# Kernel optimization log

Measured on AMD Instinct MI355X. Metric: run time of the kernel, lower is better.

## Reference

```python
import jax, jax.numpy as jnp
import numpy as np

T, B, H, W, D, N, M, A = 48, 16, 16, 48, 684, 256, 256, 512
CQ, KQ, PAD = 512, 11, 5  # coverage conv: 1->512 channels, 11x11, pad 5


def setup_inputs() -> dict:
    key = jax.random.key(0)
    ks = iter(jax.random.split(key, 40))
    w = lambda *s: jax.random.normal(next(ks), s, jnp.float32) * 0.05
    inp = {
        "embedding": jax.random.normal(next(ks), (T, B, M), jnp.float32),
        "mask": jnp.ones((T, B), jnp.float32),
        "context": jax.random.normal(next(ks), (B, D, H, W), jnp.float32),
        "context_mask": jnp.ones((B, H, W), jnp.float32),
        "init_state": jax.random.normal(next(ks), (B, N), jnp.float32),
        # attention params
        "Ua_w": w(A, D), "Ua_b": w(A),              # conv_Ua (1x1 conv == linear over channels)
        "Wa_w": w(A, N),                              # fc_Wa (no bias)
        "Q_w": w(CQ, 1, KQ, KQ),                      # conv_Q (no bias)
        "Uf_w": w(A, CQ), "Uf_b": w(A),               # fc_Uf
        "va_w": w(1, A), "va_b": w(1),                # fc_va
        # GRU 1 (input-driven)
        "Wyz_w": w(N, M), "Wyz_b": w(N),
        "Wyr_w": w(N, M), "Wyr_b": w(N),
        "Wyh_w": w(N, M), "Wyh_b": w(N),
        "Uhz_w": w(N, N), "Uhr_w": w(N, N), "Uhh_w": w(N, N),
        # GRU 2 (context-driven)
        "Wcz_w": w(N, D), "Wcr_w": w(N, D), "Wch_w": w(N, D),
        "Uhz2_w": w(N, N), "Uhz2_b": w(N),
        "Uhr2_w": w(N, N), "Uhr2_b": w(N),
        "Uhh2_w": w(N, N), "Uhh2_b": w(N),
    }
    return inp


def reference(embedding, mask, context, context_mask, init_state,
              Ua_w, Ua_b, Wa_w, Q_w, Uf_w, Uf_b, va_w, va_b,
              Wyz_w, Wyz_b, Wyr_w, Wyr_b, Wyh_w, Wyh_b,
              Uhz_w, Uhr_w, Uhh_w, Wcz_w, Wcr_w, Wch_w,
              Uhz2_w, Uhz2_b, Uhr2_w, Uhr2_b, Uhh2_w, Uhh2_b):
    # Precompute, as the torch module does, the context projection and
    # embedding projections for all steps.
    Ua_ctx = jnp.einsum('bdhw,ad->hwba', context, Ua_w) + Ua_b   # [H,W,B,A]
    sz = jnp.einsum('tbm,nm->tbn', embedding, Wyz_w) + Wyz_b     # [T,B,N]
    sr = jnp.einsum('tbm,nm->tbn', embedding, Wyr_w) + Wyr_b
    sh = jnp.einsum('tbm,nm->tbn', embedding, Wyh_w) + Wyh_b
    ctx_mask_hwb = jnp.transpose(context_mask, (1, 2, 0))        # [H,W,B]
    nb = context.shape[0]
    alpha_past0 = jnp.zeros((nb, context.shape[2], context.shape[3]), context.dtype)

    def step(carry, xs):
        h, ap = carry
        m_t, sz_t, sr_t, sh_t = xs
        # GRU 1
        z1 = jax.nn.sigmoid(h @ Uhz_w.T + sz_t)
        r1 = jax.nn.sigmoid(h @ Uhr_w.T + sr_t)
        h1p = jnp.tanh((h @ Uhh_w.T) * r1 + sh_t)
        h1 = z1 * h + (1.0 - z1) * h1p
        h1 = m_t[:, None] * h1 + (1.0 - m_t)[:, None] * h
        # coverage-conv attention
        Wa_h1 = h1 @ Wa_w.T                                      # [B,A]
        cf = jax.lax.conv_general_dilated(
            ap[:, None], Q_w, (1, 1), [(PAD, PAD), (PAD, PAD)],
            dimension_numbers=('NCHW', 'OIHW', 'NCHW'))          # [B,CQ,H,W]
        cover = jnp.einsum('bchw,ac->hwba', cf, Uf_w) + Uf_b     # [H,W,B,A]
        att = jnp.tanh(Ua_ctx + Wa_h1[None, None] + cover)
        e = jnp.einsum('hwba,a->hwb', att, va_w[0]) + va_b[0]
        alpha = jnp.exp(e) * ctx_mask_hwb
        alpha = alpha / alpha.sum(axis=(0, 1))[None, None, :]    # normalize over H,W
        a_bhw = jnp.transpose(alpha, (2, 0, 1))
        ap_new = ap + a_bhw
        ct = jnp.einsum('bdhw,bhw->bd', context, a_bhw)          # [B,D]
        # GRU 2
        z2 = jax.nn.sigmoid(ct @ Wcz_w.T + h1 @ Uhz2_w.T + Uhz2_b)
        r2 = jax.nn.sigmoid(ct @ Wcr_w.T + h1 @ Uhr2_w.T + Uhr2_b)
        h2p = jnp.tanh(ct @ Wch_w.T + (h1 @ Uhh2_w.T + Uhh2_b) * r2)
        h2 = z2 * h1 + (1.0 - z2) * h2p
        h2 = m_t[:, None] * h2 + (1.0 - m_t)[:, None] * h1
        return (h2, ap_new), (h2, ct, a_bhw, ap_new)

    _, (h2ts, cts, alphas, alpha_pasts) = jax.lax.scan(
        step, (init_state, alpha_past0), (mask, sz, sr, sh))
    return h2ts, cts, alphas, alpha_pasts
```

## Files before the change

### kernel.cpp

```cpp
#include <hip/hip_runtime.h>
#include <hip/hip_bf16.h>
#include <stdint.h>

#define T_  48
#define B_  16
#define HW_ 768
#define D_  684
#define N_  256
#define A_  512

#define OFF_SZ     0u
#define OFF_SR     196608u
#define OFF_SH     393216u
#define OFF_UHZT   589824u
#define OFF_UHZ2T  786432u
#define OFF_G2HP   983040u
#define OFF_WAT    1179648u
#define OFF_WCZT   1310720u
#define OFF_UAB    1836032u
#define OFF_WAHP   2012160u
#define OFF_H1     2077696u
#define OFF_KCB    2186240u
#define OFF_G2CT   2219008u
#define OFF_AP     2275008u
#define OFF_AUN    2287296u
#define OFF_UACTX  2299584u

#define OUT_H2 0u
#define OUT_CT 196608u
#define OUT_AL 721920u
#define OUT_AP 1311744u

typedef __attribute__((ext_vector_type(8))) short bf16x8;
typedef __attribute__((ext_vector_type(16))) float floatx16;

__device__ __forceinline__ float sigf(float x)  { return 1.f / (1.f + __expf(-x)); }
__device__ __forceinline__ float tanhf_(float x){ float e = __expf(2.f*x); return 1.f - 2.f/(e + 1.f); }
__device__ __forceinline__ float bfval(unsigned short u){ return __uint_as_float(((unsigned)u) << 16); }
__device__ __forceinline__ unsigned short f2bf(float f){
  unsigned int x = __float_as_uint(f);
  return (unsigned short)((x + 0x7fffu + ((x >> 16) & 1u)) >> 16);
}

__global__ void k_prep(const float* __restrict__ Uhz, const float* __restrict__ Uhr, const float* __restrict__ Uhh,
                       const float* __restrict__ Uhz2, const float* __restrict__ Uhr2, const float* __restrict__ Uhh2,
                       const float* __restrict__ Wyz, const float* __restrict__ Wyr, const float* __restrict__ Wyh,
                       const float* __restrict__ Wa, const float* __restrict__ Wcz, const float* __restrict__ Wcr,
                       const float* __restrict__ Wch, const float* __restrict__ Ua, float* __restrict__ ws)
{
  int i = blockIdx.x * 256 + threadIdx.x;
  if (i < 589824) {
    int m = i >> 16, rem = i & 65535, r = rem >> 8, c = rem & 255;
    const float* s;
    unsigned dst;
    switch (m) { case 0: s=Uhz;  dst=OFF_UHZT;           break;
                 case 1: s=Uhr;  dst=OFF_UHZT+65536u;    break;
                 case 2: s=Uhh;  dst=OFF_UHZT+131072u;   break;
                 case 3: s=Uhz2; dst=OFF_UHZ2T;          break;
                 case 4: s=Uhr2; dst=OFF_UHZ2T+65536u;   break;
                 case 5: s=Uhh2; dst=OFF_UHZ2T+131072u;  break;
                 case 6: s=Wyz;  dst=983040u;            break;
                 case 7: s=Wyr;  dst=1048576u;           break;
                 default: s=Wyh; dst=1114112u;           break;}
    ws[dst + c*256 + r] = s[rem];
  } else if (i < 720896) {
    int j = i - 589824, r = j >> 8, c = j & 255;
    ws[OFF_WAT + c*512 + r] = Wa[j];
  } else if (i < 1246208) {
    int j = i - 720896; int m = j / 175104; int rem = j - m*175104;
    int r = rem / 684, c = rem - r*684;
    const float* s = (m == 0) ? Wcz : (m == 1) ? Wcr : Wch;
    ws[OFF_WCZT + m*175104 + c*256 + r] = s[rem];
  } else if (i < 1596416) {
    int j = i - 1246208; int a = j / 684, d = j - a*684;
    unsigned short* uab = (unsigned short*)(ws + OFF_UAB);
    uab[(size_t)a*688 + d] = f2bf(Ua[j]);
  } else if (i < 1598464) {
    int j = i - 1596416; int a = j >> 2, d = 684 + (j & 3);
    unsigned short* uab = (unsigned short*)(ws + OFF_UAB);
    uab[(size_t)a*688 + d] = 0;
  } else if (i < 1610752) {
    ws[OFF_AP + (i - 1598464)] = 0.f;
  }
}

__global__ void __launch_bounds__(256) k_kcomb(const float* __restrict__ Uf, const float* __restrict__ Qw,
                                               float* __restrict__ ws)
{
  unsigned short* kcb = (unsigned short*)(ws + OFF_KCB);
  int tid = threadIdx.x;
  int k = tid & 127, rr = tid >> 7;
  int a = blockIdx.x * 2 + rr;
  if (k >= 121) { kcb[(size_t)a*128 + k] = 0; return; }
  const float* uf = Uf + (size_t)a*512;
  float acc = 0.f;
  #pragma unroll 8
  for (int c = 0; c < 512; ++c) acc += uf[c] * Qw[c*121 + k];
  kcb[(size_t)a*128 + k] = f2bf(acc);
}

__global__ void __launch_bounds__(256) k_embproj(const float* __restrict__ emb, const float* __restrict__ bz,
                                                 const float* __restrict__ br, const float* __restrict__ bh,
                                                 float* __restrict__ ws)
{
  __shared__ __align__(16) float s_e[256 * 16];
  __shared__ float s_part[8][32][48];
  int tid = threadIdx.x;
  int rc = blockIdx.x >> 3, cc = blockIdx.x & 7;
  int row0 = rc * 16, n0 = cc * 32;
  for (int i = tid; i < 4096; i += 256) { int r = i >> 8, m = i & 255; s_e[m*16 + r] = emb[(row0 + r)*256 + m]; }
  __syncthreads();
  int col = tid & 31, kg = tid >> 5;
  int n = n0 + col;
  float az[16], ar[16], ah[16];
  #pragma unroll
  for (int r = 0; r < 16; ++r) { az[r] = 0.f; ar[r] = 0.f; ah[r] = 0.f; }
  #pragma unroll 4
  for (int m = kg*32; m < kg*32 + 32; ++m) {
    float wz = ws[983040u + m*256 + n];
    float wr = ws[1048576u + m*256 + n];
    float wh = ws[1114112u + m*256 + n];
    const float4* ep = (const float4*)(s_e + m*16);
    #pragma unroll
    for (int rq = 0; rq < 4; ++rq) {
      float4 e4 = ep[rq];
      az[rq*4+0] += wz*e4.x; az[rq*4+1] += wz*e4.y; az[rq*4+2] += wz*e4.z; az[rq*4+3] += wz*e4.w;
      ar[rq*4+0] += wr*e4.x; ar[rq*4+1] += wr*e4.y; ar[rq*4+2] += wr*e4.z; ar[rq*4+3] += wr*e4.w;
      ah[rq*4+0] += wh*e4.x; ah[rq*4+1] += wh*e4.y; ah[rq*4+2] += wh*e4.z; ah[rq*4+3] += wh*e4.w;
    }
  }
  #pragma unroll
  for (int r = 0; r < 16; ++r) {
    s_part[kg][col][r]      = az[r];
    s_part[kg][col][16 + r] = ar[r];
    s_part[kg][col][32 + r] = ah[r];
  }
  __syncthreads();
  {
    int rcol = tid & 31, j0 = (tid >> 5) * 6;
    int rn = n0 + rcol;
    #pragma unroll
    for (int jj = 0; jj < 6; ++jj) {
      int j = j0 + jj;
      float v = 0.f;
      #pragma unroll
      for (int k8 = 0; k8 < 8; ++k8) v += s_part[k8][rcol][j];
      int g = j >> 4, r = j & 15;
      const float* bp = (g == 0) ? bz : (g == 1) ? br : bh;
      v += bp[rn];
      ws[g*196608u + (row0 + r)*256 + rn] = v;
    }
  }
}

__global__ void __launch_bounds__(256) k_uactx(const float* __restrict__ ctx, float* __restrict__ ws)
{
  __shared__ unsigned short sA[32 * 24];
  int tid = threadIdx.x;
  int blk = blockIdx.x;
  int b = blk / 48; int r2 = blk % 48; int ch = r2 >> 1; int ah = r2 & 1;
  int hw0 = ch * 32;
  const unsigned short* uab = (const unsigned short*)(ws + OFF_UAB);
  int lane = tid & 63, w = tid >> 6;
  int c5 = lane & 31, q = lane >> 5;
  int nb = ah*256 + w*64;
  floatx16 acc[2];
  #pragma unroll
  for (int nt = 0; nt < 2; ++nt)
    #pragma unroll
    for (int r = 0; r < 16; ++r) acc[nt][r] = 0.f;
  int dd = tid >> 4, iw = tid & 15;
  for (int kt = 0; kt < 43; ++kt) {
    int d = kt*16 + dd;
    float2 v = {0.f, 0.f};
    if (d < 684) v = *(const float2*)(ctx + ((size_t)(b*684 + d))*768 + hw0 + iw*2);
    __syncthreads();
    sA[(iw*2 + 0)*24 + dd] = f2bf(v.x);
    sA[(iw*2 + 1)*24 + dd] = f2bf(v.y);
    __syncthreads();
    bf16x8 af = *(const bf16x8*)(sA + c5*24 + q*8);
    #pragma unroll
    for (int nt = 0; nt < 2; ++nt) {
      bf16x8 bf = *(const bf16x8*)(uab + (size_t)(nb + nt*32 + c5)*688 + kt*16 + q*8);
      acc[nt] = __builtin_amdgcn_mfma_f32_32x32x16_bf16(af, bf, acc[nt], 0, 0, 0);
    }
  }
  unsigned short* up = (unsigned short*)(ws + OFF_UACTX);
  #pragma unroll
  for (int nt = 0; nt < 2; ++nt) {
    int col = nb + nt*32 + c5;
    #pragma unroll
    for (int r = 0; r < 16; ++r) {
      int row32 = (r & 3) + 8*(r >> 2) + 4*q;
      int hw = hw0 + row32;
      up[((size_t)(b*768 + hw))*512 + col] = f2bf(acc[nt][r]);
    }
  }
}

__global__ void __launch_bounds__(256) k_step0(const float* __restrict__ inits, const float* __restrict__ maskp,
                                               float* __restrict__ ws)
{
  __shared__ float s_h[256];
  __shared__ float s_part[3][8][32];
  __shared__ float s_h1[32];
  int tid = threadIdx.x;
  int b = blockIdx.x >> 3, q = blockIdx.x & 7;
  s_h[tid] = inits[b*256 + tid];
  if (q == 0) {
    for (int i = tid; i < 768; i += 256) ws[OFF_AUN + b*768 + i] = 0.f;
    #pragma unroll
    for (int g = 0; g < 3; ++g) ws[OFF_G2CT + (b*3 + g)*256 + tid] = 0.f;
  }
  __syncthreads();
  {
    int nl = tid & 31, kq = tid >> 5;
    int col = q*32 + nl;
    const float* Wz = ws + OFF_UHZT;
    const float* Wr = ws + OFF_UHZT + 65536u;
    const float* Wh = ws + OFF_UHZT + 131072u;
    float a0 = 0.f, a1 = 0.f, a2 = 0.f;
    #pragma unroll 8
    for (int k = kq*32; k < kq*32 + 32; ++k) {
      float hk = s_h[k];
      a0 += Wz[k*256 + col]*hk; a1 += Wr[k*256 + col]*hk; a2 += Wh[k*256 + col]*hk;
    }
    s_part[0][kq][nl] = a0; s_part[1][kq][nl] = a1; s_part[2][kq][nl] = a2;
  }
  __syncthreads();
  if (tid < 32) {
    float g0 = 0.f, g1 = 0.f, g2 = 0.f;
    #pragma unroll
    for (int j = 0; j < 8; ++j) { g0 += s_part[0][j][tid]; g1 += s_part[1][j][tid]; g2 += s_part[2][j][tid]; }
    int col = q*32 + tid;
    int ro = b*256 + col;
    float z1 = sigf(g0 + ws[OFF_SZ + ro]);
    float r1 = sigf(g1 + ws[OFF_SR + ro]);
    float h1p = tanhf_(g2 * r1 + ws[OFF_SH + ro]);
    float m = maskp[b];
    float h = s_h[col];
    float h1 = m*(z1*h + (1.f - z1)*h1p) + (1.f - m)*h;
    s_h1[tid] = h1;
    ws[OFF_H1 + b*256 + col] = h1;
  }
  __syncthreads();
  {
    float acc0 = 0.f, acc1 = 0.f;
    #pragma unroll 8
    for (int j = 0; j < 32; ++j) {
      float h1j = s_h1[j];
      acc0 += ws[OFF_WAT + (q*32 + j)*512 + tid]       * h1j;
      acc1 += ws[OFF_WAT + (q*32 + j)*512 + tid + 256] * h1j;
    }
    ws[OFF_WAHP + (size_t)(b*8 + q)*512 + tid]       = acc0;
    ws[OFF_WAHP + (size_t)(b*8 + q)*512 + tid + 256] = acc1;
  }
  #pragma unroll
  for (int g = 0; g < 3; ++g) {
    const float* Wb = ws + OFF_UHZ2T + g*65536u;
    float acc = 0.f;
    #pragma unroll 8
    for (int j = 0; j < 32; ++j) acc += Wb[(q*32 + j)*256 + tid] * s_h1[j];
    ws[OFF_G2HP + (size_t)((b*8 + q)*3 + g)*256 + tid] = acc;
  }
}

__global__ void __launch_bounds__(256) k_step1(int t, const float* __restrict__ maskp,
                                               const float* __restrict__ bz2, const float* __restrict__ br2,
                                               const float* __restrict__ bh2,
                                               float* __restrict__ out, float* __restrict__ ws)
{
  __shared__ float s_h[256];
  __shared__ float s_part[3][8][32];
  __shared__ float s_h1[32];
  int tid = threadIdx.x;
  int b = blockIdx.x >> 3, q = blockIdx.x & 7;
  const unsigned pr = (unsigned)((t - 1) & 1);
  const unsigned pw = (unsigned)(t & 1);
  {
    int n = tid;
    float h1v = ws[OFF_H1 + pr*4096u + b*256 + n];
    float gz = ws[OFF_G2CT + pr*12288u + (b*3 + 0)*256 + n];
    float gr = ws[OFF_G2CT + pr*12288u + (b*3 + 1)*256 + n];
    float gc = ws[OFF_G2CT + pr*12288u + (b*3 + 2)*256 + n];
    float gu = 0.f;
    #pragma unroll
    for (int qq = 0; qq < 8; ++qq) {
      gz += ws[OFF_G2HP + pr*98304u + (size_t)((b*8 + qq)*3 + 0)*256 + n];
      gr += ws[OFF_G2HP + pr*98304u + (size_t)((b*8 + qq)*3 + 1)*256 + n];
      gu += ws[OFF_G2HP + pr*98304u + (size_t)((b*8 + qq)*3 + 2)*256 + n];
    }
    float z2 = sigf(gz + bz2[n]);
    float r2 = sigf(gr + br2[n]);
    float h2p = tanhf_(gc + (gu + bh2[n]) * r2);
    float h2 = z2*h1v + (1.f - z2)*h2p;
    float m = maskp[(t-1)*16 + b];
    float hv = m*h2 + (1.f - m)*h1v;
    if (q == 0) out[OUT_H2 + (size_t)((t-1)*16 + b)*256 + n] = hv;
    s_h[n] = hv;
  }
  if (q == 0) {
    for (int i = tid; i < 768; i += 256) ws[OFF_AUN + b*768 + i] = 0.f;
    #pragma unroll
    for (int g = 0; g < 3; ++g) ws[OFF_G2CT + pw*12288u + (b*3 + g)*256 + tid] = 0.f;
  }
  __syncthreads();
  {
    int nl = tid & 31, kq = tid >> 5;
    int col = q*32 + nl;
    const float* Wz = ws + OFF_UHZT;
    const float* Wr = ws + OFF_UHZT + 65536u;
    const float* Wh = ws + OFF_UHZT + 131072u;
    float a0 = 0.f, a1 = 0.f, a2 = 0.f;
    #pragma unroll 8
    for (int k = kq*32; k < kq*32 + 32; ++k) {
      float hk = s_h[k];
      a0 += Wz[k*256 + col]*hk; a1 += Wr[k*256 + col]*hk; a2 += Wh[k*256 + col]*hk;
    }
    s_part[0][kq][nl] = a0; s_part[1][kq][nl] = a1; s_part[2][kq][nl] = a2;
  }
  __syncthreads();
  if (tid < 32) {
    float g0 = 0.f, g1 = 0.f, g2 = 0.f;
    #pragma unroll
    for (int j = 0; j < 8; ++j) { g0 += s_part[0][j][tid]; g1 += s_part[1][j][tid]; g2 += s_part[2][j][tid]; }
    int col = q*32 + tid;
    int ro = (t*16 + b)*256 + col;
    float z1 = sigf(g0 + ws[OFF_SZ + ro]);
    float r1 = sigf(g1 + ws[OFF_SR + ro]);
    float h1p = tanhf_(g2 * r1 + ws[OFF_SH + ro]);
    float m = maskp[t*16 + b];
    float h = s_h[col];
    float h1 = m*(z1*h + (1.f - z1)*h1p) + (1.f - m)*h;
    s_h1[tid] = h1;
    ws[OFF_H1 + pw*4096u + b*256 + col] = h1;
  }
  __syncthreads();
  {
    float acc0 = 0.f, acc1 = 0.f;
    #pragma unroll 8
    for (int j = 0; j < 32; ++j) {
      float h1j = s_h1[j];
      acc0 += ws[OFF_WAT + (q*32 + j)*512 + tid]       * h1j;
      acc1 += ws[OFF_WAT + (q*32 + j)*512 + tid + 256] * h1j;
    }
    ws[OFF_WAHP + (size_t)(b*8 + q)*512 + tid]       = acc0;
    ws[OFF_WAHP + (size_t)(b*8 + q)*512 + tid + 256] = acc1;
  }
  #pragma unroll
  for (int g = 0; g < 3; ++g) {
    const float* Wb = ws + OFF_UHZ2T + g*65536u;
    float acc = 0.f;
    #pragma unroll 8
    for (int j = 0; j < 32; ++j) acc += Wb[(q*32 + j)*256 + tid] * s_h1[j];
    ws[OFF_G2HP + pw*98304u + (size_t)((b*8 + q)*3 + g)*256 + tid] = acc;
  }
}

__global__ void __launch_bounds__(256) k_cover(const float* __restrict__ va,
                                               const float* __restrict__ Uab, const float* __restrict__ Ufb,
                                               float* __restrict__ ws)
{
  __shared__ unsigned short sA[64 * 136];
  __shared__ float sWah[512];
  __shared__ float sVa[512];
  int tid = threadIdx.x;
  int blk = blockIdx.x;
  int b = blk / 24; int chA = blk % 24; int mt = chA >> 1; int nt2 = chA & 1;
  for (int i = tid; i < 512; i += 256) {
    float v = Uab[i] + Ufb[i];
    #pragma unroll
    for (int qq = 0; qq < 8; ++qq) v += ws[OFF_WAHP + (size_t)(b*8 + qq)*512 + i];
    sWah[i] = v; sVa[i] = va[i];
  }
  const float* ap = ws + OFF_AP + b*768;
  for (int idx = tid; idx < 64*128; idx += 256) {
    int r = idx & 63, k = idx >> 6;
    int hw = mt*64 + r; int hh = hw / 48; int wwp = hw - hh*48;
    float v = 0.f;
    if (k < 121) {
      int kh = k / 11, kw = k - kh*11;
      int shh = hh + kh - 5, sww = wwp + kw - 5;
      if (shh >= 0 && shh < 16 && sww >= 0 && sww < 48) v = ap[shh*48 + sww];
    }
    sA[r*136 + k] = f2bf(v);
  }
  __syncthreads();
  int lane = tid & 63; int w = tid >> 6; int mw = w >> 1; int nw = w & 1;
  int c5 = lane & 31; int q = lane >> 5;
  bf16x8 af[8];
  {
    int m = mw*32 + c5;
    #pragma unroll
    for (int ks = 0; ks < 8; ++ks)
      af[ks] = *(const bf16x8*)(sA + m*136 + ks*16 + q*8);
  }
  const unsigned short* kct = (const unsigned short*)(ws + OFF_KCB);
  const unsigned short* uact = (const unsigned short*)(ws + OFF_UACTX);
  float e_part[16];
  #pragma unroll
  for (int r = 0; r < 16; ++r) e_part[r] = 0.f;
  for (int sp = 0; sp < 2; ++sp) {
    int n_base = nt2*256 + nw*128 + sp*64;
    floatx16 acc[2];
    #pragma unroll
    for (int r = 0; r < 16; ++r) { acc[0][r] = 0.f; acc[1][r] = 0.f; }
    const bf16x8* kb0 = (const bf16x8*)(kct + (size_t)(n_base + c5)*128 + q*8);
    const bf16x8* kb1 = (const bf16x8*)(kct + (size_t)(n_base + 32 + c5)*128 + q*8);
    #pragma unroll
    for (int ks = 0; ks < 8; ++ks) {
      bf16x8 b0 = kb0[ks*2];
      bf16x8 b1 = kb1[ks*2];
      acc[0] = __builtin_amdgcn_mfma_f32_32x32x16_bf16(af[ks], b0, acc[0], 0, 0, 0);
      acc[1] = __builtin_amdgcn_mfma_f32_32x32x16_bf16(af[ks], b1, acc[1], 0, 0, 0);
    }
    #pragma unroll
    for (int half = 0; half < 2; ++half) {
      int col = n_base + half*32 + c5;
      float vav = sVa[col], wah = sWah[col];
      #pragma unroll
      for (int r = 0; r < 16; ++r) {
        int row32 = (r & 3) + 8*(r >> 2) + 4*q;
        int hw = mt*64 + mw*32 + row32;
        float x = acc[half][r] + wah + bfval(uact[((size_t)(b*768 + hw))*512 + col]);
        e_part[r] += vav * tanhf_(x);
      }
    }
  }
  #pragma unroll
  for (int r = 0; r < 16; ++r) {
    float v = e_part[r];
    v += __shfl_xor(v, 1); v += __shfl_xor(v, 2); v += __shfl_xor(v, 4);
    v += __shfl_xor(v, 8); v += __shfl_xor(v, 16);
    e_part[r] = v;
  }
  if (c5 == 0) {
    #pragma unroll
    for (int r = 0; r < 16; ++r) {
      int row32 = (r & 3) + 8*(r >> 2) + 4*q;
      int hw = mt*64 + mw*32 + row32;
      atomicAdd(&ws[OFF_AUN + b*768 + hw], e_part[r]);
    }
  }
}

__global__ void __launch_bounds__(256) k_alpha(int t, const float* __restrict__ ctx, const float* __restrict__ cmask,
                                               const float* __restrict__ vab,
                                               float* __restrict__ out, float* __restrict__ ws)
{
  __shared__ __align__(16) float s_al[768];
  __shared__ float s_red[4];
  __shared__ float s_ct[32];
  int tid = threadIdx.x;
  int b = blockIdx.x / 22, dc = blockIdx.x % 22;
  const unsigned pw = (unsigned)(t & 1);
  float vb = vab[0];
  float local = 0.f;
  for (int i = tid; i < 768; i += 256) {
    float e = ws[OFF_AUN + b*768 + i] + vb;
    float un = __expf(e) * cmask[b*768 + i];
    s_al[i] = un; local += un;
  }
  local += __shfl_xor(local, 1); local += __shfl_xor(local, 2); local += __shfl_xor(local, 4);
  local += __shfl_xor(local, 8); local += __shfl_xor(local, 16); local += __shfl_xor(local, 32);
  if ((tid & 63) == 0) s_red[tid >> 6] = local;
  __syncthreads();
  float inv = 1.f / (s_red[0] + s_red[1] + s_red[2] + s_red[3]);
  if (dc == 0) {
    float* outA = out + OUT_AL + (size_t)(t*16 + b)*768;
    float* outP = out + OUT_AP + (size_t)(t*16 + b)*768;
    for (int i = tid; i < 768; i += 256) {
      float av = s_al[i] * inv;
      float np = ws[OFF_AP + b*768 + i] + av;
      ws[OFF_AP + b*768 + i] = np;
      outA[i] = av; outP[i] = np;
    }
  }
  {
    int dl = tid >> 3, qq = tid & 7;
    int d = dc*32 + dl;
    if (d < 684) {
      const float4* cp  = (const float4*)(ctx + ((size_t)(b*684 + d))*768);
      const float4* alp = (const float4*)s_al;
      float s = 0.f;
      #pragma unroll 8
      for (int i = 0; i < 24; ++i) {
        float4 cv = cp[i*8 + qq]; float4 av = alp[i*8 + qq];
        s += cv.x*av.x + cv.y*av.y + cv.z*av.z + cv.w*av.w;
      }
      s += __shfl_xor(s, 1); s += __shfl_xor(s, 2); s += __shfl_xor(s, 4);
      s *= inv;
      if (qq == 0) {
        out[OUT_CT + (size_t)(t*16 + b)*684 + d] = s;
        s_ct[dl] = s;
      }
    } else if (qq == 0) {
      s_ct[dl] = 0.f;
    }
  }
  __syncthreads();
  {
    int d0 = dc*32;
    int jm = 684 - d0; if (jm > 32) jm = 32;
    #pragma unroll
    for (int g = 0; g < 3; ++g) {
      const float* Wb = ws + OFF_WCZT + g*175104u;
      float acc = 0.f;
      for (int j = 0; j < jm; ++j) acc += Wb[(d0 + j)*256 + tid] * s_ct[j];
      atomicAdd(&ws[OFF_G2CT + pw*12288u + (size_t)(b*3 + g)*256 + tid], acc);
    }
  }
}

__global__ void k_final(const float* __restrict__ maskp, const float* __restrict__ bz2,
                        const float* __restrict__ br2, const float* __restrict__ bh2,
                        float* __restrict__ out, float* __restrict__ ws)
{
  int b = blockIdx.x, n = threadIdx.x;
  const unsigned pr = 1u;
  float h1v = ws[OFF_H1 + pr*4096u + b*256 + n];
  float gz = ws[OFF_G2CT + pr*12288u + (b*3 + 0)*256 + n];
  float gr = ws[OFF_G2CT + pr*12288u + (b*3 + 1)*256 + n];
  float gc = ws[OFF_G2CT + pr*12288u + (b*3 + 2)*256 + n];
  float gu = 0.f;
  #pragma unroll
  for (int qq = 0; qq < 8; ++qq) {
    gz += ws[OFF_G2HP + pr*98304u + (size_t)((b*8 + qq)*3 + 0)*256 + n];
    gr += ws[OFF_G2HP + pr*98304u + (size_t)((b*8 + qq)*3 + 1)*256 + n];
    gu += ws[OFF_G2HP + pr*98304u + (size_t)((b*8 + qq)*3 + 2)*256 + n];
  }
  float z2 = sigf(gz + bz2[n]);
  float r2 = sigf(gr + br2[n]);
  float h2p = tanhf_(gc + (gu + bh2[n]) * r2);
  float h2 = z2*h1v + (1.f - z2)*h2p;
  float m = maskp[47*16 + b];
  out[OUT_H2 + (size_t)(47*16 + b)*256 + n] = m*h2 + (1.f - m)*h1v;
}

extern "C" void kernel_launch(void* const* d_in, const int* in_sizes, int n_in,
                              void* d_out, int out_size, void* d_ws, size_t ws_size,
                              hipStream_t stream)
{
  const float* emb   = (const float*)d_in[0];
  const float* maskp = (const float*)d_in[1];
  const float* ctx   = (const float*)d_in[2];
  const float* cmask = (const float*)d_in[3];
  const float* inits = (const float*)d_in[4];
  const float* Ua    = (const float*)d_in[5];
  const float* Uab   = (const float*)d_in[6];
  const float* Wa    = (const float*)d_in[7];
  const float* Qw    = (const float*)d_in[8];
  const float* Uf    = (const float*)d_in[9];
  const float* Ufb   = (const float*)d_in[10];
  const float* va    = (const float*)d_in[11];
  const float* vab   = (const float*)d_in[12];
  const float* Wyz   = (const float*)d_in[13];
  const float* Wyzb  = (const float*)d_in[14];
  const float* Wyr   = (const float*)d_in[15];
  const float* Wyrb  = (const float*)d_in[16];
  const float* Wyh   = (const float*)d_in[17];
  const float* Wyhb  = (const float*)d_in[18];
  const float* Uhz   = (const float*)d_in[19];
  const float* Uhr   = (const float*)d_in[20];
  const float* Uhh   = (const float*)d_in[21];
  const float* Wcz   = (const float*)d_in[22];
  const float* Wcr   = (const float*)d_in[23];
  const float* Wch   = (const float*)d_in[24];
  const float* Uhz2  = (const float*)d_in[25];
  const float* Uhz2b = (const float*)d_in[26];
  const float* Uhr2  = (const float*)d_in[27];
  const float* Uhr2b = (const float*)d_in[28];
  const float* Uhh2  = (const float*)d_in[29];
  const float* Uhh2b = (const float*)d_in[30];
  float* out = (float*)d_out;
  float* ws  = (float*)d_ws;

  k_prep<<<dim3(6292), dim3(256), 0, stream>>>(Uhz, Uhr, Uhh, Uhz2, Uhr2, Uhh2,
                                               Wyz, Wyr, Wyh, Wa, Wcz, Wcr, Wch, Ua, ws);
  k_kcomb<<<dim3(256), dim3(256), 0, stream>>>(Uf, Qw, ws);
  k_embproj<<<dim3(384), dim3(256), 0, stream>>>(emb, Wyzb, Wyrb, Wyhb, ws);
  k_uactx<<<dim3(768), dim3(256), 0, stream>>>(ctx, ws);
  k_step0<<<dim3(128), dim3(256), 0, stream>>>(inits, maskp, ws);

  k_cover<<<dim3(384), dim3(256), 0, stream>>>(va, Uab, Ufb, ws);
  k_alpha<<<dim3(352), dim3(256), 0, stream>>>(0, ctx, cmask, vab, out, ws);
  for (int t = 1; t < 48; ++t) {
    k_step1<<<dim3(128), dim3(256), 0, stream>>>(t, maskp, Uhz2b, Uhr2b, Uhh2b, out, ws);
    k_cover<<<dim3(384), dim3(256), 0, stream>>>(va, Uab, Ufb, ws);
    k_alpha<<<dim3(352), dim3(256), 0, stream>>>(t, ctx, cmask, vab, out, ws);
  }
  k_final<<<dim3(16), dim3(256), 0, stream>>>(maskp, Uhz2b, Uhr2b, Uhh2b, out, ws);
  (void)in_sizes; (void)n_in; (void)out_size; (void)ws_size;
}
```

Measured before the change: 2.473 ms.

## Fuse per-step kernels into one persistent kernel with per-batch grid barriers

Replaces the 144 per-timestep kernel launches (step, cover, alpha) with a single persistent kernel of 384 blocks. Each batch element gets 24 blocks, and they synchronize through an atomic counter barrier in workspace between phases. This removes launch overhead and the full-device serialization between dependent kernels. The risks are deadlock if not all blocks are co-resident, spin-wait cost, and idle blocks in phases that use only 8 or 22 of the 24 blocks.

Measured after the change: 6.602 ms. 167% more time.

```diff
diff --git a/kernel.cpp b/kernel.cpp
--- a/kernel.cpp
+++ b/kernel.cpp
@@ -20,6 +20,7 @@
 #define OFF_UAB    1836032u
 #define OFF_WAHP   2012160u
 #define OFF_H1     2077696u
+#define OFF_BAR    2085888u
 #define OFF_KCB    2186240u
 #define OFF_G2CT   2219008u
 #define OFF_AP     2275008u
@@ -81,6 +82,8 @@
     uab[(size_t)a*688 + d] = 0;
   } else if (i < 1610752) {
     ws[OFF_AP + (i - 1598464)] = 0.f;
+  } else if (i < 1611008) {
+    ws[OFF_BAR + (i - 1610752)] = 0.f;
   }
 }
 
@@ -198,87 +201,275 @@
   }
 }
 
-__global__ void __launch_bounds__(256) k_step0(const float* __restrict__ inits, const float* __restrict__ maskp,
-                                               float* __restrict__ ws)
+__global__ void __launch_bounds__(256, 2) k_loop(
+    const float* __restrict__ inits, const float* __restrict__ maskp,
+    const float* __restrict__ bz2, const float* __restrict__ br2, const float* __restrict__ bh2,
+    const float* __restrict__ va, const float* __restrict__ Uab, const float* __restrict__ Ufb,
+    const float* __restrict__ ctx, const float* __restrict__ cmask, const float* __restrict__ vab,
+    float* __restrict__ out, float* ws)
 {
-  __shared__ float s_h[256];
-  __shared__ float s_part[3][8][32];
-  __shared__ float s_h1[32];
+  __shared__ union {
+    struct { float s_h[256]; float s_part[3][8][32]; float s_h1[32]; } p1;
+    struct { unsigned short sA[64*136]; float sWah[512]; float sVa[512]; } p2;
+    struct { __align__(16) float s_al[768]; float s_red[4]; float s_ct[32]; } p3;
+  } u;
   int tid = threadIdx.x;
-  int b = blockIdx.x >> 3, q = blockIdx.x & 7;
-  s_h[tid] = inits[b*256 + tid];
-  if (q == 0) {
-    for (int i = tid; i < 768; i += 256) ws[OFF_AUN + b*768 + i] = 0.f;
-    #pragma unroll
-    for (int g = 0; g < 3; ++g) ws[OFF_G2CT + (b*3 + g)*256 + tid] = 0.f;
-  }
-  __syncthreads();
-  {
-    int nl = tid & 31, kq = tid >> 5;
-    int col = q*32 + nl;
-    const float* Wz = ws + OFF_UHZT;
-    const float* Wr = ws + OFF_UHZT + 65536u;
-    const float* Wh = ws + OFF_UHZT + 131072u;
-    float a0 = 0.f, a1 = 0.f, a2 = 0.f;
-    #pragma unroll 8
-    for (int k = kq*32; k < kq*32 + 32; ++k) {
-      float hk = s_h[k];
-      a0 += Wz[k*256 + col]*hk; a1 += Wr[k*256 + col]*hk; a2 += Wh[k*256 + col]*hk;
-    }
-    s_part[0][kq][nl] = a0; s_part[1][kq][nl] = a1; s_part[2][kq][nl] = a2;
-  }
-  __syncthreads();
-  if (tid < 32) {
-    float g0 = 0.f, g1 = 0.f, g2 = 0.f;
-    #pragma unroll
-    for (int j = 0; j < 8; ++j) { g0 += s_part[0][j][tid]; g1 += s_part[1][j][tid]; g2 += s_part[2][j][tid]; }
-    int col = q*32 + tid;
-    int ro = b*256 + col;
-    float z1 = sigf(g0 + ws[OFF_SZ + ro]);
-    float r1 = sigf(g1 + ws[OFF_SR + ro]);
-    float h1p = tanhf_(g2 * r1 + ws[OFF_SH + ro]);
-    float m = maskp[b];
-    float h = s_h[col];
-    float h1 = m*(z1*h + (1.f - z1)*h1p) + (1.f - m)*h;
-    s_h1[tid] = h1;
-    ws[OFF_H1 + b*256 + col] = h1;
-  }
-  __syncthreads();
-  {
-    float acc0 = 0.f, acc1 = 0.f;
-    #pragma unroll 8
-    for (int j = 0; j < 32; ++j) {
-      float h1j = s_h1[j];
-      acc0 += ws[OFF_WAT + (q*32 + j)*512 + tid]       * h1j;
-      acc1 += ws[OFF_WAT + (q*32 + j)*512 + tid + 256] * h1j;
-    }
-    ws[OFF_WAHP + (size_t)(b*8 + q)*512 + tid]       = acc0;
-    ws[OFF_WAHP + (size_t)(b*8 + q)*512 + tid + 256] = acc1;
-  }
-  #pragma unroll
-  for (int g = 0; g < 3; ++g) {
-    const float* Wb = ws + OFF_UHZ2T + g*65536u;
-    float acc = 0.f;
-    #pragma unroll 8
-    for (int j = 0; j < 32; ++j) acc += Wb[(q*32 + j)*256 + tid] * s_h1[j];
-    ws[OFF_G2HP + (size_t)((b*8 + q)*3 + g)*256 + tid] = acc;
-  }
-}
-
-__global__ void __launch_bounds__(256) k_step1(int t, const float* __restrict__ maskp,
-                                               const float* __restrict__ bz2, const float* __restrict__ br2,
-                                               const float* __restrict__ bh2,
-                                               float* __restrict__ out, float* __restrict__ ws)
-{
-  __shared__ float s_h[256];
-  __shared__ float s_part[3][8][32];
-  __shared__ float s_h1[32];
-  int tid = threadIdx.x;
-  int b = blockIdx.x >> 3, q = blockIdx.x & 7;
-  const unsigned pr = (unsigned)((t - 1) & 1);
-  const unsigned pw = (unsigned)(t & 1);
-  {
+  int b = blockIdx.x / 24, j = blockIdx.x % 24;
+  unsigned* bar = (unsigned*)(ws + OFF_BAR) + b*16;
+  unsigned bk = 0;
+
+#define GBAR() do { \
+    __syncthreads(); \
+    if (tid == 0) { \
+      __threadfence(); \
+      __hip_atomic_fetch_add(bar, 1u, __ATOMIC_RELAXED, __HIP_MEMORY_SCOPE_AGENT); \
+      bk += 24u; \
+      while (__hip_atomic_load(bar, __ATOMIC_RELAXED, __HIP_MEMORY_SCOPE_AGENT) < bk) \
+        __builtin_amdgcn_s_sleep(4); \
+      __threadfence(); \
+    } \
+    __syncthreads(); \
+  } while (0)
+
+  for (int t = 0; t < 48; ++t) {
+    if (j < 8) {
+      int q = j;
+      if (t == 0) {
+        u.p1.s_h[tid] = inits[b*256 + tid];
+        if (q == 0) {
+          for (int i = tid; i < 768; i += 256) ws[OFF_AUN + b*768 + i] = 0.f;
+          #pragma unroll
+          for (int g = 0; g < 3; ++g) ws[OFF_G2CT + (b*3 + g)*256 + tid] = 0.f;
+        }
+        __syncthreads();
+      } else {
+        const unsigned pr = (unsigned)((t - 1) & 1);
+        const unsigned pw = (unsigned)(t & 1);
+        {
+          int n = tid;
+          float h1v = ws[OFF_H1 + pr*4096u + b*256 + n];
+          float gz = ws[OFF_G2CT + pr*12288u + (b*3 + 0)*256 + n];
+          float gr = ws[OFF_G2CT + pr*12288u + (b*3 + 1)*256 + n];
+          float gc = ws[OFF_G2CT + pr*12288u + (b*3 + 2)*256 + n];
+          float gu = 0.f;
+          #pragma unroll
+          for (int qq = 0; qq < 8; ++qq) {
+            gz += ws[OFF_G2HP + pr*98304u + (size_t)((b*8 + qq)*3 + 0)*256 + n];
+            gr += ws[OFF_G2HP + pr*98304u + (size_t)((b*8 + qq)*3 + 1)*256 + n];
+            gu += ws[OFF_G2HP + pr*98304u + (size_t)((b*8 + qq)*3 + 2)*256 + n];
+          }
+          float z2 = sigf(gz + bz2[n]);
+          float r2 = sigf(gr + br2[n]);
+          float h2p = tanhf_(gc + (gu + bh2[n]) * r2);
+          float h2 = z2*h1v + (1.f - z2)*h2p;
+          float m = maskp[(t-1)*16 + b];
+          float hv = m*h2 + (1.f - m)*h1v;
+          if (q == 0) out[OUT_H2 + (size_t)((t-1)*16 + b)*256 + n] = hv;
+          u.p1.s_h[n] = hv;
+        }
+        if (q == 0) {
+          for (int i = tid; i < 768; i += 256) ws[OFF_AUN + b*768 + i] = 0.f;
+          #pragma unroll
+          for (int g = 0; g < 3; ++g) ws[OFF_G2CT + pw*12288u + (b*3 + g)*256 + tid] = 0.f;
+        }
+        __syncthreads();
+      }
+      {
+        int nl = tid & 31, kq = tid >> 5;
+        int col = q*32 + nl;
+        const float* Wz = ws + OFF_UHZT;
+        const float* Wr = ws + OFF_UHZT + 65536u;
+        const float* Wh = ws + OFF_UHZT + 131072u;
+        float a0 = 0.f, a1 = 0.f, a2 = 0.f;
+        #pragma unroll 8
+        for (int k = kq*32; k < kq*32 + 32; ++k) {
+          float hk = u.p1.s_h[k];
+          a0 += Wz[k*256 + col]*hk; a1 += Wr[k*256 + col]*hk; a2 += Wh[k*256 + col]*hk;
+        }
+        u.p1.s_part[0][kq][nl] = a0; u.p1.s_part[1][kq][nl] = a1; u.p1.s_part[2][kq][nl] = a2;
+      }
+      __syncthreads();
+      if (tid < 32) {
+        float g0 = 0.f, g1 = 0.f, g2 = 0.f;
+        #pragma unroll
+        for (int jj = 0; jj < 8; ++jj) { g0 += u.p1.s_part[0][jj][tid]; g1 += u.p1.s_part[1][jj][tid]; g2 += u.p1.s_part[2][jj][tid]; }
+        int col = q*32 + tid;
+        int ro = (t*16 + b)*256 + col;
+        float z1 = sigf(g0 + ws[OFF_SZ + ro]);
+        float r1 = sigf(g1 + ws[OFF_SR + ro]);
+        float h1p = tanhf_(g2 * r1 + ws[OFF_SH + ro]);
+        float m = maskp[t*16 + b];
+        float h = u.p1.s_h[col];
+        float h1 = m*(z1*h + (1.f - z1)*h1p) + (1.f - m)*h;
+        u.p1.s_h1[tid] = h1;
+        ws[OFF_H1 + (unsigned)(t & 1)*4096u + b*256 + col] = h1;
+      }
+      __syncthreads();
+      {
+        float acc0 = 0.f, acc1 = 0.f;
+        #pragma unroll 8
+        for (int jj = 0; jj < 32; ++jj) {
+          float h1j = u.p1.s_h1[jj];
+          acc0 += ws[OFF_WAT + (q*32 + jj)*512 + tid]       * h1j;
+          acc1 += ws[OFF_WAT + (q*32 + jj)*512 + tid + 256] * h1j;
+        }
+        ws[OFF_WAHP + (size_t)(b*8 + q)*512 + tid]       = acc0;
+        ws[OFF_WAHP + (size_t)(b*8 + q)*512 + tid + 256] = acc1;
+      }
+      #pragma unroll
+      for (int g = 0; g < 3; ++g) {
+        const float* Wb = ws + OFF_UHZ2T + g*65536u;
+        float acc = 0.f;
+        #pragma unroll 8
+        for (int jj = 0; jj < 32; ++jj) acc += Wb[(q*32 + jj)*256 + tid] * u.p1.s_h1[jj];
+        ws[OFF_G2HP + (unsigned)(t & 1)*98304u + (size_t)((b*8 + q)*3 + g)*256 + tid] = acc;
+      }
+    }
+    GBAR();
+    {
+      int mt = j >> 1, nt2 = j & 1;
+      for (int i = tid; i < 512; i += 256) {
+        float v = Uab[i] + Ufb[i];
+        #pragma unroll
+        for (int qq = 0; qq < 8; ++qq) v += ws[OFF_WAHP + (size_t)(b*8 + qq)*512 + i];
+        u.p2.sWah[i] = v; u.p2.sVa[i] = va[i];
+      }
+      const float* ap = ws + OFF_AP + b*768;
+      for (int idx = tid; idx < 64*128; idx += 256) {
+        int r = idx & 63, k = idx >> 6;
+        int hw = mt*64 + r; int hh = hw / 48; int wwp = hw - hh*48;
+        float v = 0.f;
+        if (k < 121) {
+          int kh = k / 11, kw = k - kh*11;
+          int shh = hh + kh - 5, sww = wwp + kw - 5;
+          if (shh >= 0 && shh < 16 && sww >= 0 && sww < 48) v = ap[shh*48 + sww];
+        }
+        u.p2.sA[r*136 + k] = f2bf(v);
+      }
+      __syncthreads();
+      int lane = tid & 63; int w = tid >> 6; int mw = w >> 1; int nw = w & 1;
+      int c5 = lane & 31; int q = lane >> 5;
+      bf16x8 af[8];
+      {
+        int m = mw*32 + c5;
+        #pragma unroll
+        for (int ks = 0; ks < 8; ++ks)
+          af[ks] = *(const bf16x8*)(u.p2.sA + m*136 + ks*16 + q*8);
+      }
+      const unsigned short* kct = (const unsigned short*)(ws + OFF_KCB);
+      const unsigned short* uact = (const unsigned short*)(ws + OFF_UACTX);
+      float e_part[16];
+      #pragma unroll
+      for (int r = 0; r < 16; ++r) e_part[r] = 0.f;
+      for (int sp = 0; sp < 2; ++sp) {
+        int n_base = nt2*256 + nw*128 + sp*64;
+        floatx16 acc[2];
+        #pragma unroll
+        for (int r = 0; r < 16; ++r) { acc[0][r] = 0.f; acc[1][r] = 0.f; }
+        const bf16x8* kb0 = (const bf16x8*)(kct + (size_t)(n_base + c5)*128 + q*8);
+        const bf16x8* kb1 = (const bf16x8*)(kct + (size_t)(n_base + 32 + c5)*128 + q*8);
+        #pragma unroll
+        for (int ks = 0; ks < 8; ++ks) {
+          bf16x8 b0 = kb0[ks*2];
+          bf16x8 b1 = kb1[ks*2];
+          acc[0] = __builtin_amdgcn_mfma_f32_32x32x16_bf16(af[ks], b0, acc[0], 0, 0, 0);
+          acc[1] = __builtin_amdgcn_mfma_f32_32x32x16_bf16(af[ks], b1, acc[1], 0, 0, 0);
+        }
+        #pragma unroll
+        for (int half = 0; half < 2; ++half) {
+          int col = n_base + half*32 + c5;
+          float vav = u.p2.sVa[col], wah = u.p2.sWah[col];
+          #pragma unroll
+          for (int r = 0; r < 16; ++r) {
+            int row32 = (r & 3) + 8*(r >> 2) + 4*q;
+            int hw = mt*64 + mw*32 + row32;
+            float x = acc[half][r] + wah + bfval(uact[((size_t)(b*768 + hw))*512 + col]);
+            e_part[r] += vav * tanhf_(x);
+          }
+        }
+      }
+      #pragma unroll
+      for (int r = 0; r < 16; ++r) {
+        float v = e_part[r];
+        v += __shfl_xor(v, 1); v += __shfl_xor(v, 2); v += __shfl_xor(v, 4);
+        v += __shfl_xor(v, 8); v += __shfl_xor(v, 16);
+        e_part[r] = v;
+      }
+      if (c5 == 0) {
+        #pragma unroll
+        for (int r = 0; r < 16; ++r) {
+          int row32 = (r & 3) + 8*(r >> 2) + 4*q;
+          int hw = mt*64 + mw*32 + row32;
+          atomicAdd(&ws[OFF_AUN + b*768 + hw], e_part[r]);
+        }
+      }
+    }
+    GBAR();
+    if (j < 22) {
+      int dc = j;
+      const unsigned pw = (unsigned)(t & 1);
+      float vb = vab[0];
+      float local = 0.f;
+      for (int i = tid; i < 768; i += 256) {
+        float e = ws[OFF_AUN + b*768 + i] + vb;
+        float un = __expf(e) * cmask[b*768 + i];
+        u.p3.s_al[i] = un; local += un;
+      }
+      local += __shfl_xor(local, 1); local += __shfl_xor(local, 2); local += __shfl_xor(local, 4);
+      local += __shfl_xor(local, 8); local += __shfl_xor(local, 16); local += __shfl_xor(local, 32);
+      if ((tid & 63) == 0) u.p3.s_red[tid >> 6] = local;
+      __syncthreads();
+      float inv = 1.f / (u.p3.s_red[0] + u.p3.s_red[1] + u.p3.s_red[2] + u.p3.s_red[3]);
+      if (dc == 0) {
+        float* outA = out + OUT_AL + (size_t)(t*16 + b)*768;
+        float* outP = out + OUT_AP + (size_t)(t*16 + b)*768;
+        for (int i = tid; i < 768; i += 256) {
+          float av = u.p3.s_al[i] * inv;
+          float np = ws[OFF_AP + b*768 + i] + av;
+          ws[OFF_AP + b*768 + i] = np;
+          outA[i] = av; outP[i] = np;
+        }
+      }
+      {
+        int dl = tid >> 3, qq = tid & 7;
+        int d = dc*32 + dl;
+        if (d < 684) {
+          const float4* cp  = (const float4*)(ctx + ((size_t)(b*684 + d))*768);
+          const float4* alp = (const float4*)u.p3.s_al;
+          float s = 0.f;
+          #pragma unroll 8
+          for (int i = 0; i < 24; ++i) {
+            float4 cv = cp[i*8 + qq]; float4 av = alp[i*8 + qq];
+            s += cv.x*av.x + cv.y*av.y + cv.z*av.z + cv.w*av.w;
+          }
+          s += __shfl_xor(s, 1); s += __shfl_xor(s, 2); s += __shfl_xor(s, 4);
+          s *= inv;
+          if (qq == 0) {
+            out[OUT_CT + (size_t)(t*16 + b)*684 + d] = s;
+            u.p3.s_ct[dl] = s;
+          }
+        } else if (qq == 0) {
+          u.p3.s_ct[dl] = 0.f;
+        }
+      }
+      __syncthreads();
+      {
+        int d0 = dc*32;
+        int jm = 684 - d0; if (jm > 32) jm = 32;
+        #pragma unroll
+        for (int g = 0; g < 3; ++g) {
+          const float* Wb = ws + OFF_WCZT + g*175104u;
+          float acc = 0.f;
+          for (int jj = 0; jj < jm; ++jj) acc += Wb[(d0 + jj)*256 + tid] * u.p3.s_ct[jj];
+          atomicAdd(&ws[OFF_G2CT + pw*12288u + (size_t)(b*3 + g)*256 + tid], acc);
+        }
+      }
+    }
+    GBAR();
+  }
+  if (j == 0) {
     int n = tid;
+    const unsigned pr = 1u;
     float h1v = ws[OFF_H1 + pr*4096u + b*256 + n];
     float gz = ws[OFF_G2CT + pr*12288u + (b*3 + 0)*256 + n];
     float gr = ws[OFF_G2CT + pr*12288u + (b*3 + 1)*256 + n];
@@ -294,247 +485,10 @@
     float r2 = sigf(gr + br2[n]);
     float h2p = tanhf_(gc + (gu + bh2[n]) * r2);
     float h2 = z2*h1v + (1.f - z2)*h2p;
-    float m = maskp[(t-1)*16 + b];
-    float hv = m*h2 + (1.f - m)*h1v;
-    if (q == 0) out[OUT_H2 + (size_t)((t-1)*16 + b)*256 + n] = hv;
-    s_h[n] = hv;
-  }
-  if (q == 0) {
-    for (int i = tid; i < 768; i += 256) ws[OFF_AUN + b*768 + i] = 0.f;
-    #pragma unroll
-    for (int g = 0; g < 3; ++g) ws[OFF_G2CT + pw*12288u + (b*3 + g)*256 + tid] = 0.f;
-  }
-  __syncthreads();
-  {
-    int nl = tid & 31, kq = tid >> 5;
-    int col = q*32 + nl;
-    const float* Wz = ws + OFF_UHZT;
-    const float* Wr = ws + OFF_UHZT + 65536u;
-    const float* Wh = ws + OFF_UHZT + 131072u;
-    float a0 = 0.f, a1 = 0.f, a2 = 0.f;
-    #pragma unroll 8
-    for (int k = kq*32; k < kq*32 + 32; ++k) {
-      float hk = s_h[k];
-      a0 += Wz[k*256 + col]*hk; a1 += Wr[k*256 + col]*hk; a2 += Wh[k*256 + col]*hk;
-    }
-    s_part[0][kq][nl] = a0; s_part[1][kq][nl] = a1; s_part[2][kq][nl] = a2;
-  }
-  __syncthreads();
-  if (tid < 32) {
-    float g0 = 0.f, g1 = 0.f, g2 = 0.f;
-    #pragma unroll
-    for (int j = 0; j < 8; ++j) { g0 += s_part[0][j][tid]; g1 += s_part[1][j][tid]; g2 += s_part[2][j][tid]; }
-    int col = q*32 + tid;
-    int ro = (t*16 + b)*256 + col;
-    float z1 = sigf(g0 + ws[OFF_SZ + ro]);
-    float r1 = sigf(g1 + ws[OFF_SR + ro]);
-    float h1p = tanhf_(g2 * r1 + ws[OFF_SH + ro]);
-    float m = maskp[t*16 + b];
-    float h = s_h[col];
-    float h1 = m*(z1*h + (1.f - z1)*h1p) + (1.f - m)*h;
-    s_h1[tid] = h1;
-    ws[OFF_H1 + pw*4096u + b*256 + col] = h1;
-  }
-  __syncthreads();
-  {
-    float acc0 = 0.f, acc1 = 0.f;
-    #pragma unroll 8
-    for (int j = 0; j < 32; ++j) {
-      float h1j = s_h1[j];
-      acc0 += ws[OFF_WAT + (q*32 + j)*512 + tid]       * h1j;
-      acc1 += ws[OFF_WAT + (q*32 + j)*512 + tid + 256] * h1j;
-    }
-    ws[OFF_WAHP + (size_t)(b*8 + q)*512 + tid]       = acc0;
-    ws[OFF_WAHP + (size_t)(b*8 + q)*512 + tid + 256] = acc1;
-  }
-  #pragma unroll
-  for (int g = 0; g < 3; ++g) {
-    const float* Wb = ws + OFF_UHZ2T + g*65536u;
-    float acc = 0.f;
-    #pragma unroll 8
-    for (int j = 0; j < 32; ++j) acc += Wb[(q*32 + j)*256 + tid] * s_h1[j];
-    ws[OFF_G2HP + pw*98304u + (size_t)((b*8 + q)*3 + g)*256 + tid] = acc;
-  }
-}
-
-__global__ void __launch_bounds__(256) k_cover(const float* __restrict__ va,
-                                               const float* __restrict__ Uab, const float* __restrict__ Ufb,
-                                               float* __restrict__ ws)
-{
-  __shared__ unsigned short sA[64 * 136];
-  __shared__ float sWah[512];
-  __shared__ float sVa[512];
-  int tid = threadIdx.x;
-  int blk = blockIdx.x;
-  int b = blk / 24; int chA = blk % 24; int mt = chA >> 1; int nt2 = chA & 1;
-  for (int i = tid; i < 512; i += 256) {
-    float v = Uab[i] + Ufb[i];
-    #pragma unroll
-    for (int qq = 0; qq < 8; ++qq) v += ws[OFF_WAHP + (size_t)(b*8 + qq)*512 + i];
-    sWah[i] = v; sVa[i] = va[i];
-  }
-  const float* ap = ws + OFF_AP + b*768;
-  for (int idx = tid; idx < 64*128; idx += 256) {
-    int r = idx & 63, k = idx >> 6;
-    int hw = mt*64 + r; int hh = hw / 48; int wwp = hw - hh*48;
-    float v = 0.f;
-    if (k < 121) {
-      int kh = k / 11, kw = k - kh*11;
-      int shh = hh + kh - 5, sww = wwp + kw - 5;
-      if (shh >= 0 && shh < 16 && sww >= 0 && sww < 48) v = ap[shh*48 + sww];
-    }
-    sA[r*136 + k] = f2bf(v);
-  }
-  __syncthreads();
-  int lane = tid & 63; int w = tid >> 6; int mw = w >> 1; int nw = w & 1;
-  int c5 = lane & 31; int q = lane >> 5;
-  bf16x8 af[8];
-  {
-    int m = mw*32 + c5;
-    #pragma unroll
-    for (int ks = 0; ks < 8; ++ks)
-      af[ks] = *(const bf16x8*)(sA + m*136 + ks*16 + q*8);
-  }
-  const unsigned short* kct = (const unsigned short*)(ws + OFF_KCB);
-  const unsigned short* uact = (const unsigned short*)(ws + OFF_UACTX);
-  float e_part[16];
-  #pragma unroll
-  for (int r = 0; r < 16; ++r) e_part[r] = 0.f;
-  for (int sp = 0; sp < 2; ++sp) {
-    int n_base = nt2*256 + nw*128 + sp*64;
-    floatx16 acc[2];
-    #pragma unroll
-    for (int r = 0; r < 16; ++r) { acc[0][r] = 0.f; acc[1][r] = 0.f; }
-    const bf16x8* kb0 = (const bf16x8*)(kct + (size_t)(n_base + c5)*128 + q*8);
-    const bf16x8* kb1 = (const bf16x8*)(kct + (size_t)(n_base + 32 + c5)*128 + q*8);
-    #pragma unroll
-    for (int ks = 0; ks < 8; ++ks) {
-      bf16x8 b0 = kb0[ks*2];
-      bf16x8 b1 = kb1[ks*2];
-      acc[0] = __builtin_amdgcn_mfma_f32_32x32x16_bf16(af[ks], b0, acc[0], 0, 0, 0);
-      acc[1] = __builtin_amdgcn_mfma_f32_32x32x16_bf16(af[ks], b1, acc[1], 0, 0, 0);
-    }
-    #pragma unroll
-    for (int half = 0; half < 2; ++half) {
-      int col = n_base + half*32 + c5;
-      float vav = sVa[col], wah = sWah[col];
-      #pragma unroll
-      for (int r = 0; r < 16; ++r) {
-        int row32 = (r & 3) + 8*(r >> 2) + 4*q;
-        int hw = mt*64 + mw*32 + row32;
-        float x = acc[half][r] + wah + bfval(uact[((size_t)(b*768 + hw))*512 + col]);
-        e_part[r] += vav * tanhf_(x);
-      }
-    }
-  }
-  #pragma unroll
-  for (int r = 0; r < 16; ++r) {
-    float v = e_part[r];
-    v += __shfl_xor(v, 1); v += __shfl_xor(v, 2); v += __shfl_xor(v, 4);
-    v += __shfl_xor(v, 8); v += __shfl_xor(v, 16);
-    e_part[r] = v;
-  }
-  if (c5 == 0) {
-    #pragma unroll
-    for (int r = 0; r < 16; ++r) {
-      int row32 = (r & 3) + 8*(r >> 2) + 4*q;
-      int hw = mt*64 + mw*32 + row32;
-      atomicAdd(&ws[OFF_AUN + b*768 + hw], e_part[r]);
-    }
-  }
-}
-
-__global__ void __launch_bounds__(256) k_alpha(int t, const float* __restrict__ ctx, const float* __restrict__ cmask,
-                                               const float* __restrict__ vab,
-                                               float* __restrict__ out, float* __restrict__ ws)
-{
-  __shared__ __align__(16) float s_al[768];
-  __shared__ float s_red[4];
-  __shared__ float s_ct[32];
-  int tid = threadIdx.x;
-  int b = blockIdx.x / 22, dc = blockIdx.x % 22;
-  const unsigned pw = (unsigned)(t & 1);
-  float vb = vab[0];
-  float local = 0.f;
-  for (int i = tid; i < 768; i += 256) {
-    float e = ws[OFF_AUN + b*768 + i] + vb;
-    float un = __expf(e) * cmask[b*768 + i];
-    s_al[i] = un; local += un;
-  }
-  local += __shfl_xor(local, 1); local += __shfl_xor(local, 2); local += __shfl_xor(local, 4);
-  local += __shfl_xor(local, 8); local += __shfl_xor(local, 16); local += __shfl_xor(local, 32);
-  if ((tid & 63) == 0) s_red[tid >> 6] = local;
-  __syncthreads();
-  float inv = 1.f / (s_red[0] + s_red[1] + s_red[2] + s_red[3]);
-  if (dc == 0) {
-    float* outA = out + OUT_AL + (size_t)(t*16 + b)*768;
-    float* outP = out + OUT_AP + (size_t)(t*16 + b)*768;
-    for (int i = tid; i < 768; i += 256) {
-      float av = s_al[i] * inv;
-      float np = ws[OFF_AP + b*768 + i] + av;
-      ws[OFF_AP + b*768 + i] = np;
-      outA[i] = av; outP[i] = np;
-    }
-  }
-  {
-    int dl = tid >> 3, qq = tid & 7;
-    int d = dc*32 + dl;
-    if (d < 684) {
-      const float4* cp  = (const float4*)(ctx + ((size_t)(b*684 + d))*768);
-      const float4* alp = (const float4*)s_al;
-      float s = 0.f;
-      #pragma unroll 8
-      for (int i = 0; i < 24; ++i) {
-        float4 cv = cp[i*8 + qq]; float4 av = alp[i*8 + qq];
-        s += cv.x*av.x + cv.y*av.y + cv.z*av.z + cv.w*av.w;
-      }
-      s += __shfl_xor(s, 1); s += __shfl_xor(s, 2); s += __shfl_xor(s, 4);
-      s *= inv;
-      if (qq == 0) {
-        out[OUT_CT + (size_t)(t*16 + b)*684 + d] = s;
-        s_ct[dl] = s;
-      }
-    } else if (qq == 0) {
-      s_ct[dl] = 0.f;
-    }
-  }
-  __syncthreads();
-  {
-    int d0 = dc*32;
-    int jm = 684 - d0; if (jm > 32) jm = 32;
-    #pragma unroll
-    for (int g = 0; g < 3; ++g) {
-      const float* Wb = ws + OFF_WCZT + g*175104u;
-      float acc = 0.f;
-      for (int j = 0; j < jm; ++j) acc += Wb[(d0 + j)*256 + tid] * s_ct[j];
-      atomicAdd(&ws[OFF_G2CT + pw*12288u + (size_t)(b*3 + g)*256 + tid], acc);
-    }
-  }
-}
-
-__global__ void k_final(const float* __restrict__ maskp, const float* __restrict__ bz2,
-                        const float* __restrict__ br2, const float* __restrict__ bh2,
-                        float* __restrict__ out, float* __restrict__ ws)
-{
-  int b = blockIdx.x, n = threadIdx.x;
-  const unsigned pr = 1u;
-  float h1v = ws[OFF_H1 + pr*4096u + b*256 + n];
-  float gz = ws[OFF_G2CT + pr*12288u + (b*3 + 0)*256 + n];
-  float gr = ws[OFF_G2CT + pr*12288u + (b*3 + 1)*256 + n];
-  float gc = ws[OFF_G2CT + pr*12288u + (b*3 + 2)*256 + n];
-  float gu = 0.f;
-  #pragma unroll
-  for (int qq = 0; qq < 8; ++qq) {
-    gz += ws[OFF_G2HP + pr*98304u + (size_t)((b*8 + qq)*3 + 0)*256 + n];
-    gr += ws[OFF_G2HP + pr*98304u + (size_t)((b*8 + qq)*3 + 1)*256 + n];
-    gu += ws[OFF_G2HP + pr*98304u + (size_t)((b*8 + qq)*3 + 2)*256 + n];
-  }
-  float z2 = sigf(gz + bz2[n]);
-  float r2 = sigf(gr + br2[n]);
-  float h2p = tanhf_(gc + (gu + bh2[n]) * r2);
-  float h2 = z2*h1v + (1.f - z2)*h2p;
-  float m = maskp[47*16 + b];
-  out[OUT_H2 + (size_t)(47*16 + b)*256 + n] = m*h2 + (1.f - m)*h1v;
+    float m = maskp[47*16 + b];
+    out[OUT_H2 + (size_t)(47*16 + b)*256 + n] = m*h2 + (1.f - m)*h1v;
+  }
+#undef GBAR
 }
 
 extern "C" void kernel_launch(void* const* d_in, const int* in_sizes, int n_in,
@@ -575,20 +529,12 @@
   float* out = (float*)d_out;
   float* ws  = (float*)d_ws;
 
-  k_prep<<<dim3(6292), dim3(256), 0, stream>>>(Uhz, Uhr, Uhh, Uhz2, Uhr2, Uhh2,
+  k_prep<<<dim3(6293), dim3(256), 0, stream>>>(Uhz, Uhr, Uhh, Uhz2, Uhr2, Uhh2,
                                                Wyz, Wyr, Wyh, Wa, Wcz, Wcr, Wch, Ua, ws);
   k_kcomb<<<dim3(256), dim3(256), 0, stream>>>(Uf, Qw, ws);
   k_embproj<<<dim3(384), dim3(256), 0, stream>>>(emb, Wyzb, Wyrb, Wyhb, ws);
   k_uactx<<<dim3(768), dim3(256), 0, stream>>>(ctx, ws);
-  k_step0<<<dim3(128), dim3(256), 0, stream>>>(inits, maskp, ws);
-
-  k_cover<<<dim3(384), dim3(256), 0, stream>>>(va, Uab, Ufb, ws);
-  k_alpha<<<dim3(352), dim3(256), 0, stream>>>(0, ctx, cmask, vab, out, ws);
-  for (int t = 1; t < 48; ++t) {
-    k_step1<<<dim3(128), dim3(256), 0, stream>>>(t, maskp, Uhz2b, Uhr2b, Uhh2b, out, ws);
-    k_cover<<<dim3(384), dim3(256), 0, stream>>>(va, Uab, Ufb, ws);
-    k_alpha<<<dim3(352), dim3(256), 0, stream>>>(t, ctx, cmask, vab, out, ws);
-  }
-  k_final<<<dim3(16), dim3(256), 0, stream>>>(maskp, Uhz2b, Uhr2b, Uhh2b, out, ws);
+  k_loop<<<dim3(384), dim3(256), 0, stream>>>(inits, maskp, Uhz2b, Uhr2b, Uhh2b,
+                                              va, Uab, Ufb, ctx, cmask, vab, out, ws);
   (void)in_sizes; (void)n_in; (void)out_size; (void)ws_size;
 }
```
